# Kernel tuning notes

Hardware: AMD Instinct MI355X
Metric: run time of the kernel (lower is better)

Reference implementation:

```python
import jax, jax.numpy as jnp
import numpy as np

CG_ITER = 10

def _fftc(x):
    # centered orthonormal 2D FFT over last two axes
    ax = (-2, -1)
    return jnp.fft.fftshift(jnp.fft.fft2(jnp.fft.ifftshift(x, axes=ax), axes=ax, norm='ortho'), axes=ax)

def _ifftc(x):
    ax = (-2, -1)
    return jnp.fft.fftshift(jnp.fft.ifft2(jnp.fft.ifftshift(x, axes=ax), axes=ax, norm='ortho'), axes=ax)

def setup_inputs() -> dict:
    key = jax.random.key(0)
    k1, k2, k3, k4, k5 = jax.random.split(key, 5)
    B, C, H, W = 8, 16, 320, 320
    us_image = jax.random.normal(k1, (B, 2, H, W), dtype=jnp.float32)
    reconstruction = jax.random.normal(k2, (B, 2, H, W), dtype=jnp.float32)
    mask = (jax.random.uniform(k3, (B, 1, H, W)) < 0.4).astype(jnp.float32)
    csm_r = jax.random.normal(k4, (B, C, H, W), dtype=jnp.float32)
    csm_i = jax.random.normal(k5, (B, C, H, W), dtype=jnp.float32)
    mu = jnp.full((1,), 0.5, dtype=jnp.float32)
    return {'us_image': us_image, 'reconstruction': reconstruction, 'mask': mask,
            'csm_r': csm_r, 'csm_i': csm_i, 'mu': mu}

def reference(us_image, reconstruction, mask, csm_r, csm_i, mu):
    csm = csm_r + 1j * csm_i                      # [B,C,H,W] complex64
    m = mu[0]
    r = (us_image[:, 0] + 1j * us_image[:, 1]) + m * (reconstruction[:, 0] + 1j * reconstruction[:, 1])  # [B,H,W]
    p = r
    b = jnp.zeros_like(r)
    for _ in range(CG_ITER):
        coil_p = p[:, None, :, :] * csm           # coil projection [B,C,H,W]
        kspace = _fftc(coil_p) * mask             # masked k-space
        q = jnp.sum(_ifftc(kspace) * jnp.conj(csm), axis=1) + m * p  # coil combine + Tikhonov
        rr = jnp.sum(r * jnp.conj(r))
        alpha = rr / jnp.sum(q * jnp.conj(p))
        b = b + alpha * p
        r_new = r - alpha * q
        beta = jnp.sum(r_new * jnp.conj(r_new)) / rr
        p = r_new + beta * p
        r = r_new
    return jnp.stack((b.real, b.imag), axis=1).astype(jnp.float32)  # [B,2,H,W]
```

## Files before the change

### kernel.cpp

```cpp
#include <hip/hip_runtime.h>

#define HW2 320
#define NB 8
#define NC 16
#define NPIX (HW2*HW2)
#define NVEC (NB*NPIX)
#define CGI 10
#define FSCALE (1.0f/102400.0f)

__device__ inline float2 cadd(float2 a, float2 b){return make_float2(a.x+b.x, a.y+b.y);}
__device__ inline float2 csub(float2 a, float2 b){return make_float2(a.x-b.x, a.y-b.y);}
__device__ inline float2 cmul(float2 a, float2 b){return make_float2(a.x*b.x-a.y*b.y, a.x*b.y+a.y*b.x);}
__device__ inline float2 cmulc(float2 a, float2 b){return make_float2(a.x*b.x+a.y*b.y, a.y*b.x-a.x*b.y);}
__device__ inline float2 cscale(float2 a, float s){return make_float2(a.x*s, a.y*s);}
__device__ inline int rev6(int t){ return (int)(__brev((unsigned)t) >> 26); }
__device__ inline float2 shflx2(float2 a, int m){ return make_float2(__shfl_xor(a.x,m,64), __shfl_xor(a.y,m,64)); }
__device__ inline float2 shfl2(float2 a, int l){ return make_float2(__shfl(a.x,l,64), __shfl(a.y,l,64)); }

template<int H>
__device__ inline float2 xsh2t(float2 a) {
  if constexpr (H == 1) {
    return make_float2(
      __int_as_float(__builtin_amdgcn_mov_dpp(__float_as_int(a.x), 0xB1, 0xF, 0xF, true)),
      __int_as_float(__builtin_amdgcn_mov_dpp(__float_as_int(a.y), 0xB1, 0xF, 0xF, true)));
  } else if constexpr (H == 2) {
    return make_float2(
      __int_as_float(__builtin_amdgcn_mov_dpp(__float_as_int(a.x), 0x4E, 0xF, 0xF, true)),
      __int_as_float(__builtin_amdgcn_mov_dpp(__float_as_int(a.y), 0x4E, 0xF, 0xF, true)));
  } else if constexpr (H == 32) {
    return shflx2(a, 32);
  } else {
    constexpr int imm = (H << 10) | 0x1F;
    return make_float2(
      __int_as_float(__builtin_amdgcn_ds_swizzle(__float_as_int(a.x), imm)),
      __int_as_float(__builtin_amdgcn_ds_swizzle(__float_as_int(a.y), imm)));
  }
}

template<int DIR>
__device__ inline void radix5(float2 (&v)[5]) {
  const float c1 = 0.30901699437494745f, s1 = 0.9510565162951535f;
  const float c2 = -0.8090169943749473f, s2 = 0.5877852522924731f;
  float2 t1 = cadd(v[1], v[4]), t2 = csub(v[1], v[4]);
  float2 t3 = cadd(v[2], v[3]), t4 = csub(v[2], v[3]);
  float2 y0 = cadd(v[0], cadd(t1, t3));
  float2 a1 = make_float2(v[0].x + c1*t1.x + c2*t3.x, v[0].y + c1*t1.y + c2*t3.y);
  float2 a2 = make_float2(v[0].x + c2*t1.x + c1*t3.x, v[0].y + c2*t1.y + c1*t3.y);
  float2 b1 = make_float2(s1*t2.x + s2*t4.x, s1*t2.y + s2*t4.y);
  float2 b2 = make_float2(s2*t2.x - s1*t4.x, s2*t2.y - s1*t4.y);
  const float sg = (float)DIR;
  float2 ib1 = make_float2(-sg*b1.y, sg*b1.x);
  float2 ib2 = make_float2(-sg*b2.y, sg*b2.x);
  v[0] = y0;
  v[1] = cadd(a1, ib1); v[4] = csub(a1, ib1);
  v[2] = cadd(a2, ib2); v[3] = csub(a2, ib2);
}

__device__ inline void load_tw(const float2* __restrict__ twg, int t,
                               float2 (&tw5)[4], float2 (&Wf)[6], float (&sg)[6]) {
  #pragma unroll
  for (int q = 1; q < 5; ++q) tw5[q-1] = twg[q*t];
  float2 tw[6];
  tw[0] = twg[5*(t&31)];
  tw[1] = twg[10*(t&15)];
  tw[2] = twg[20*(t&7)];
  tw[3] = twg[40*(t&3)];
  tw[4] = twg[80*(t&1)];
  tw[5] = make_float2(1.f, 0.f);
  #pragma unroll
  for (int s = 0; s < 6; ++s) {
    bool up = (t & (32 >> s)) != 0;
    Wf[s] = up ? tw[s] : make_float2(1.f, 0.f);
    sg[s] = up ? -1.f : 1.f;
  }
}

template<int H, int NCOL>
__device__ inline void bf_fwd(float2 (&v)[NCOL][5], float2 w, float st) {
  #pragma unroll
  for (int q = 0; q < 5; ++q)
    #pragma unroll
    for (int k = 0; k < NCOL; ++k) {
      float2 o = xsh2t<H>(v[k][q]);
      float2 tmp = make_float2(fmaf(st, v[k][q].x, o.x), fmaf(st, v[k][q].y, o.y));
      v[k][q] = cmul(tmp, w);
    }
}
template<int H, int NCOL>
__device__ inline void bf_inv(float2 (&v)[NCOL][5], float2 w, float st) {
  #pragma unroll
  for (int q = 0; q < 5; ++q)
    #pragma unroll
    for (int k = 0; k < NCOL; ++k) {
      float2 mine = cmulc(v[k][q], w);
      float2 o = xsh2t<H>(mine);
      v[k][q] = make_float2(fmaf(st, mine.x, o.x), fmaf(st, mine.y, o.y));
    }
}

template<int NCOL>
__device__ inline void fft320_fwd_r(float2 (&v)[NCOL][5],
                                    const float2 (&tw5)[4], const float2 (&Wf)[6],
                                    const float (&sg)[6]) {
  #pragma unroll
  for (int k = 0; k < NCOL; ++k) radix5<-1>(v[k]);
  #pragma unroll
  for (int q = 1; q < 5; ++q)
    #pragma unroll
    for (int k = 0; k < NCOL; ++k) v[k][q] = cmul(v[k][q], tw5[q-1]);
  bf_fwd<32>(v, Wf[0], sg[0]);
  bf_fwd<16>(v, Wf[1], sg[1]);
  bf_fwd< 8>(v, Wf[2], sg[2]);
  bf_fwd< 4>(v, Wf[3], sg[3]);
  bf_fwd< 2>(v, Wf[4], sg[4]);
  bf_fwd< 1>(v, Wf[5], sg[5]);
}
template<int NCOL>
__device__ inline void fft320_inv_r(float2 (&v)[NCOL][5],
                                    const float2 (&tw5)[4], const float2 (&Wf)[6],
                                    const float (&sg)[6]) {
  bf_inv< 1>(v, Wf[5], sg[5]);
  bf_inv< 2>(v, Wf[4], sg[4]);
  bf_inv< 4>(v, Wf[3], sg[3]);
  bf_inv< 8>(v, Wf[2], sg[2]);
  bf_inv<16>(v, Wf[1], sg[1]);
  bf_inv<32>(v, Wf[0], sg[0]);
  #pragma unroll
  for (int q = 1; q < 5; ++q)
    #pragma unroll
    for (int k = 0; k < NCOL; ++k) v[k][q] = cmulc(v[k][q], tw5[q-1]);
  #pragma unroll
  for (int k = 0; k < NCOL; ++k) radix5<1>(v[k]);
}

__global__ void k_twiddle(float2* tw) {
  int m = blockIdx.x*blockDim.x + threadIdx.x;
  if (m < 320) {
    double a = -2.0 * 3.14159265358979323846 * (double)m / 320.0;
    tw[m] = make_float2((float)cos(a), (float)sin(a));
  }
}

__global__ void k_init(const float* __restrict__ us, const float* __restrict__ rec,
                       const float* __restrict__ mu,
                       float2* r, float2* p, float2* bv) {
  int i = blockIdx.x*blockDim.x + threadIdx.x;
  if (i >= NVEC) return;
  float m = mu[0];
  int b = i / NPIX, hw = i % NPIX;
  float re = us[(size_t)(b*2+0)*NPIX + hw] + m * rec[(size_t)(b*2+0)*NPIX + hw];
  float im = us[(size_t)(b*2+1)*NPIX + hw] + m * rec[(size_t)(b*2+1)*NPIX + hw];
  float2 v = make_float2(re, im);
  r[i] = v; p[i] = v; bv[i] = make_float2(0.f, 0.f);
}

__global__ __launch_bounds__(256) void k_proj_rowfft(
    const float2* __restrict__ pv, const float* __restrict__ csr,
    const float* __restrict__ csi, float2* __restrict__ K,
    const float2* __restrict__ twg, int b0) {
  __shared__ float2 stage[8][320];
  int t = threadIdx.x & 63, w = threadIdx.x >> 6, rt = rev6(t);
  float2 tw5[4], Wf[6]; float sg[6];
  load_tw(twg, t, tw5, Wf, sg);
  int wid = blockIdx.x*4 + w;
  int rp  = wid % (HW2/2);
  int c   = (wid / (HW2/2)) % NC;
  int bl  = wid / ((HW2/2)*NC);
  int b   = b0 + bl;
  int row0 = rp*2;
  const float2* prow = pv + ((size_t)(b*HW2) + row0)*HW2;
  size_t cs = ((size_t)((b*NC + c)*HW2) + row0)*HW2;
  float sgn0 = ((row0 + t) & 1) ? -1.f : 1.f;
  float sgn1 = -sgn0;
  float2 v[2][5];
  #pragma unroll
  for (int j = 0; j < 5; ++j) {
    int n = t + 64*j;
    float2 cv0 = make_float2(csr[cs+n],     csi[cs+n]);
    float2 cv1 = make_float2(csr[cs+HW2+n], csi[cs+HW2+n]);
    v[0][j] = cscale(cmul(prow[n],     cv0), sgn0);
    v[1][j] = cscale(cmul(prow[HW2+n], cv1), sgn1);
  }
  fft320_fwd_r<2>(v, tw5, Wf, sg);
  #pragma unroll
  for (int q = 0; q < 5; ++q) {
    stage[w*2+0][5*rt + q] = v[0][q];
    stage[w*2+1][5*rt + q] = v[1][q];
  }
  float2* Krow = K + ((size_t)((bl*NC + c)*HW2) + row0)*HW2;
  #pragma unroll
  for (int j = 0; j < 5; ++j) {
    Krow[t + 64*j]       = stage[w*2+0][t + 64*j];
    Krow[HW2 + t + 64*j] = stage[w*2+1][t + 64*j];
  }
}

__global__ __launch_bounds__(512, 4) void k_colfft_mask(
    float2* __restrict__ K, const float* __restrict__ mask,
    const float2* __restrict__ twg, int b0) {
  __shared__ float re[320][17];
  __shared__ float im[320][17];
  __shared__ unsigned char mk8[320][20];
  int tile = blockIdx.x % 20;
  int c    = (blockIdx.x/20) % NC;
  int bl   = blockIdx.x/(20*NC);
  int b    = b0 + bl;
  float2* Kimg = K + (size_t)(bl*NC + c)*NPIX;
  const float4* Kimg4 = (const float4*)Kimg;
  const float4* Mimg4 = (const float4*)(mask + (size_t)b*NPIX);
  int t = threadIdx.x & 63, w = threadIdx.x >> 6, rt = rev6(t);
  float2 tw5[4], Wf[6]; float sg[6];
  load_tw(twg, t, tw5, Wf, sg);
  for (int idx = threadIdx.x; idx < 320*8; idx += 512) {
    int rw = idx >> 3, c4 = idx & 7;
    float4 v4 = Kimg4[(size_t)rw*160 + tile*8 + c4];
    re[rw][2*c4+0] = v4.x; im[rw][2*c4+0] = v4.y;
    re[rw][2*c4+1] = v4.z; im[rw][2*c4+1] = v4.w;
  }
  for (int idx = threadIdx.x; idx < 320*4; idx += 512) {
    int rw = idx >> 2, c4 = idx & 3;
    float4 m4 = Mimg4[(size_t)rw*80 + tile*4 + c4];
    mk8[rw][4*c4+0] = (unsigned char)(m4.x != 0.f);
    mk8[rw][4*c4+1] = (unsigned char)(m4.y != 0.f);
    mk8[rw][4*c4+2] = (unsigned char)(m4.z != 0.f);
    mk8[rw][4*c4+3] = (unsigned char)(m4.w != 0.f);
  }
  __syncthreads();
  const int colA = w*2, colB = w*2 + 1;
  float2 v[2][5];
  #pragma unroll
  for (int j = 0; j < 5; ++j) {
    v[0][j] = make_float2(re[t+64*j][colA], im[t+64*j][colA]);
    v[1][j] = make_float2(re[t+64*j][colB], im[t+64*j][colB]);
  }
  fft320_fwd_r<2>(v, tw5, Wf, sg);
  #pragma unroll
  for (int q = 0; q < 5; ++q) {
    int rowk = 5*rt + q;
    float m0 = mk8[rowk][colA] ? FSCALE : 0.f;
    float m1 = mk8[rowk][colB] ? FSCALE : 0.f;
    v[0][q] = cscale(v[0][q], m0);
    v[1][q] = cscale(v[1][q], m1);
  }
  fft320_inv_r<2>(v, tw5, Wf, sg);
  #pragma unroll
  for (int j = 0; j < 5; ++j) {
    re[t+64*j][colA] = v[0][j].x; im[t+64*j][colA] = v[0][j].y;
    re[t+64*j][colB] = v[1][j].x; im[t+64*j][colB] = v[1][j].y;
  }
  __syncthreads();
  float4* Kimg4w = (float4*)Kimg;
  for (int idx = threadIdx.x; idx < 320*8; idx += 512) {
    int rw = idx >> 3, c4 = idx & 7;
    float4 v4;
    v4.x = re[rw][2*c4+0]; v4.y = im[rw][2*c4+0];
    v4.z = re[rw][2*c4+1]; v4.w = im[rw][2*c4+1];
    Kimg4w[(size_t)rw*160 + tile*8 + c4] = v4;
  }
}

__global__ __launch_bounds__(256) void k_irowfft_combine(
    const float2* __restrict__ K, const float* __restrict__ csr,
    const float* __restrict__ csi, const float2* __restrict__ pv,
    float2* __restrict__ qv, const float* __restrict__ mu,
    const float2* __restrict__ twg, int b0) {
  __shared__ float2 rows[4][320];
  int t = threadIdx.x & 63, w = threadIdx.x >> 6, rt = rev6(t);
  float2 tw5[4], Wf[6]; float sg[6];
  load_tw(twg, t, tw5, Wf, sg);
  int row = blockIdx.x % HW2;
  int bl  = blockIdx.x / HW2;
  int b   = b0 + bl;
  float sgn = ((row + t) & 1) ? -1.f : 1.f;
  float2 acc[5];
  #pragma unroll
  for (int j = 0; j < 5; ++j) acc[j] = make_float2(0.f, 0.f);
  #pragma unroll
  for (int half = 0; half < 2; ++half) {
    int c0 = w + 8*half;
    const float2* Kr0 = K + ((size_t)((bl*NC + c0)*HW2) + row)*HW2;
    const float2* Kr1 = Kr0 + (size_t)4*NPIX;
    float2 v[2][5];
    #pragma unroll
    for (int q = 0; q < 5; ++q) { v[0][q] = Kr0[5*t+q]; v[1][q] = Kr1[5*t+q]; }
    #pragma unroll
    for (int q = 0; q < 5; ++q) { v[0][q] = shfl2(v[0][q], rt); v[1][q] = shfl2(v[1][q], rt); }
    fft320_inv_r<2>(v, tw5, Wf, sg);
    size_t cs0 = ((size_t)((b*NC + c0)*HW2) + row)*HW2;
    size_t cs1 = cs0 + (size_t)4*NPIX;
    #pragma unroll
    for (int j = 0; j < 5; ++j) {
      int n = t + 64*j;
      float2 cv0 = make_float2(csr[cs0+n], csi[cs0+n]);
      float2 cv1 = make_float2(csr[cs1+n], csi[cs1+n]);
      acc[j] = cadd(acc[j], cadd(cmulc(v[0][j], cv0), cmulc(v[1][j], cv1)));
    }
  }
  #pragma unroll
  for (int j = 0; j < 5; ++j) rows[w][t+64*j] = cscale(acc[j], sgn);
  __syncthreads();
  float m = mu[0];
  const float* pf = (const float*)(pv + ((size_t)(b*HW2) + row)*HW2);
  float*       qf = (float*)(qv + ((size_t)(b*HW2) + row)*HW2);
  const float* rf = (const float*)rows;
  for (int i = threadIdx.x; i < 640; i += 256) {
    float s = rf[i] + rf[640+i] + rf[1280+i] + rf[1920+i];
    qf[i] = s + m * pf[i];
  }
}

__global__ void k_dot_rr(const float4* __restrict__ r, float2* partials) {
  float s = 0.f;
  for (int i = blockIdx.x*blockDim.x + threadIdx.x; i < NVEC/2; i += gridDim.x*blockDim.x) {
    float4 v = r[i]; s += v.x*v.x + v.y*v.y + v.z*v.z + v.w*v.w;
  }
  __shared__ float buf[4];
  for (int off = 32; off; off >>= 1) s += __shfl_down(s, off, 64);
  int w = threadIdx.x >> 6, t = threadIdx.x & 63;
  if (t == 0) buf[w] = s;
  __syncthreads();
  if (threadIdx.x == 0) partials[blockIdx.x] = make_float2(buf[0]+buf[1]+buf[2]+buf[3], 0.f);
}
__global__ void k_rr_finish(const float2* __restrict__ partials, float2* scal) {
  float s = 0.f;
  for (int i = threadIdx.x; i < 256; i += blockDim.x) s += partials[i].x;
  __shared__ float buf[4];
  for (int off = 32; off; off >>= 1) s += __shfl_down(s, off, 64);
  int w = threadIdx.x >> 6, t = threadIdx.x & 63;
  if (t == 0) buf[w] = s;
  __syncthreads();
  if (threadIdx.x == 0) scal[0] = make_float2(buf[0]+buf[1]+buf[2]+buf[3], 0.f);
}
__global__ void k_dot_pq(const float4* __restrict__ q, const float4* __restrict__ p, float2* partials) {
  float sr = 0.f, si = 0.f;
  for (int i = blockIdx.x*blockDim.x + threadIdx.x; i < NVEC/2; i += gridDim.x*blockDim.x) {
    float4 qq = q[i], pp = p[i];
    sr += qq.x*pp.x + qq.y*pp.y + qq.z*pp.z + qq.w*pp.w;
    si += qq.y*pp.x - qq.x*pp.y + qq.w*pp.z - qq.z*pp.w;
  }
  __shared__ float2 buf[4];
  for (int off = 32; off; off >>= 1) { sr += __shfl_down(sr, off, 64); si += __shfl_down(si, off, 64); }
  int w = threadIdx.x >> 6, t = threadIdx.x & 63;
  if (t == 0) buf[w] = make_float2(sr, si);
  __syncthreads();
  if (threadIdx.x == 0)
    partials[blockIdx.x] = make_float2(buf[0].x+buf[1].x+buf[2].x+buf[3].x,
                                       buf[0].y+buf[1].y+buf[2].y+buf[3].y);
}
__global__ void k_alpha(const float2* __restrict__ partials, float2* scal) {
  float sr = 0.f, si = 0.f;
  for (int i = threadIdx.x; i < 256; i += blockDim.x) { sr += partials[i].x; si += partials[i].y; }
  __shared__ float2 buf[4];
  for (int off = 32; off; off >>= 1) { sr += __shfl_down(sr, off, 64); si += __shfl_down(si, off, 64); }
  int w = threadIdx.x >> 6, t = threadIdx.x & 63;
  if (t == 0) buf[w] = make_float2(sr, si);
  __syncthreads();
  if (threadIdx.x == 0) {
    float pr = buf[0].x+buf[1].x+buf[2].x+buf[3].x;
    float pi = buf[0].y+buf[1].y+buf[2].y+buf[3].y;
    float rr = scal[0].x;
    float d = pr*pr + pi*pi;
    scal[1] = make_float2(rr*pr/d, -rr*pi/d);
  }
}
__global__ void k_update(float4* bv, float4* r, const float4* __restrict__ p,
                         const float4* __restrict__ q, const float2* __restrict__ scal,
                         float2* partials) {
  float2 al = scal[1];
  float s = 0.f;
  for (int i = blockIdx.x*blockDim.x + threadIdx.x; i < NVEC/2; i += gridDim.x*blockDim.x) {
    float4 pp = p[i], qq = q[i], bb = bv[i], rr = r[i];
    bb.x += al.x*pp.x - al.y*pp.y;  bb.y += al.x*pp.y + al.y*pp.x;
    bb.z += al.x*pp.z - al.y*pp.w;  bb.w += al.x*pp.w + al.y*pp.z;
    bv[i] = bb;
    rr.x -= al.x*qq.x - al.y*qq.y;  rr.y -= al.x*qq.y + al.y*qq.x;
    rr.z -= al.x*qq.z - al.y*qq.w;  rr.w -= al.x*qq.w + al.y*qq.z;
    r[i] = rr;
    s += rr.x*rr.x + rr.y*rr.y + rr.z*rr.z + rr.w*rr.w;
  }
  __shared__ float buf[4];
  for (int off = 32; off; off >>= 1) s += __shfl_down(s, off, 64);
  int w = threadIdx.x >> 6, t = threadIdx.x & 63;
  if (t == 0) buf[w] = s;
  __syncthreads();
  if (threadIdx.x == 0) partials[blockIdx.x] = make_float2(buf[0]+buf[1]+buf[2]+buf[3], 0.f);
}
__global__ void k_beta(const float2* __restrict__ partials, float2* scal) {
  float s = 0.f;
  for (int i = threadIdx.x; i < 256; i += blockDim.x) s += partials[i].x;
  __shared__ float buf[4];
  for (int off = 32; off; off >>= 1) s += __shfl_down(s, off, 64);
  int w = threadIdx.x >> 6, t = threadIdx.x & 63;
  if (t == 0) buf[w] = s;
  __syncthreads();
  if (threadIdx.x == 0) {
    float rrnew = buf[0]+buf[1]+buf[2]+buf[3];
    float rrold = scal[0].x;
    scal[2] = make_float2(rrnew/rrold, 0.f);
    scal[0] = make_float2(rrnew, 0.f);
  }
}
__global__ void k_pupdate(float4* p, const float4* __restrict__ r, const float2* __restrict__ scal) {
  float be = scal[2].x;
  for (int i = blockIdx.x*blockDim.x + threadIdx.x; i < NVEC/2; i += gridDim.x*blockDim.x) {
    float4 pp = p[i], rr = r[i];
    pp.x = rr.x + be*pp.x; pp.y = rr.y + be*pp.y;
    pp.z = rr.z + be*pp.z; pp.w = rr.w + be*pp.w;
    p[i] = pp;
  }
}
__global__ void k_output(const float2* __restrict__ bv, float* __restrict__ out) {
  int i = blockIdx.x*blockDim.x + threadIdx.x;
  if (i >= NVEC) return;
  int b = i / NPIX, hw = i % NPIX;
  float2 v = bv[i];
  out[(size_t)(b*2+0)*NPIX + hw] = v.x;
  out[(size_t)(b*2+1)*NPIX + hw] = v.y;
}

extern "C" void kernel_launch(void* const* d_in, const int* in_sizes, int n_in,
                              void* d_out, int out_size, void* d_ws, size_t ws_size,
                              hipStream_t stream) {
  const float* us  = (const float*)d_in[0];
  const float* rec = (const float*)d_in[1];
  const float* msk = (const float*)d_in[2];
  const float* csr = (const float*)d_in[3];
  const float* csi = (const float*)d_in[4];
  const float* mu  = (const float*)d_in[5];
  float* out = (float*)d_out;

  const size_t vecB = (size_t)NVEC * 8;
  int nb = NB;
  while (nb > 1 && ((size_t)nb*NC*NPIX*8 + 4*vecB + 320*8 + 256*8 + 64) > ws_size) nb >>= 1;

  char* w = (char*)d_ws; size_t off = 0;
  float2* K        = (float2*)(w + off); off += (size_t)nb*NC*NPIX*8;
  float2* rv       = (float2*)(w + off); off += vecB;
  float2* pv       = (float2*)(w + off); off += vecB;
  float2* bv       = (float2*)(w + off); off += vecB;
  float2* qv       = (float2*)(w + off); off += vecB;
  float2* twg      = (float2*)(w + off); off += 320*8;
  float2* partials = (float2*)(w + off); off += 256*8;
  float2* scal     = (float2*)(w + off);

  k_twiddle<<<dim3(2), dim3(256), 0, stream>>>(twg);
  k_init<<<dim3(NVEC/256), dim3(256), 0, stream>>>(us, rec, mu, rv, pv, bv);
  k_dot_rr<<<dim3(256), dim3(256), 0, stream>>>((const float4*)rv, partials);
  k_rr_finish<<<dim3(1), dim3(256), 0, stream>>>(partials, scal);

  for (int it = 0; it < CGI; ++it) {
    for (int b0 = 0; b0 < NB; b0 += nb) {
      k_proj_rowfft    <<<dim3(nb*NC*(HW2/2)/4), dim3(256), 0, stream>>>(pv, csr, csi, K, twg, b0);
      k_colfft_mask    <<<dim3(nb*NC*20),        dim3(512), 0, stream>>>(K, msk, twg, b0);
      k_irowfft_combine<<<dim3(nb*HW2),          dim3(256), 0, stream>>>(K, csr, csi, pv, qv, mu, twg, b0);
    }
    k_dot_pq <<<dim3(256), dim3(256), 0, stream>>>((const float4*)qv, (const float4*)pv, partials);
    k_alpha  <<<dim3(1),   dim3(256), 0, stream>>>(partials, scal);
    k_update <<<dim3(256), dim3(256), 0, stream>>>((float4*)bv, (float4*)rv, (const float4*)pv,
                                                   (const float4*)qv, scal, partials);
    k_beta   <<<dim3(1),   dim3(256), 0, stream>>>(partials, scal);
    k_pupdate<<<dim3(256), dim3(256), 0, stream>>>((float4*)pv, (const float4*)rv, scal);
  }
  k_output<<<dim3(NVEC/256), dim3(256), 0, stream>>>(bv, out);
}
```

Before: 1.618 ms.

## Keep k-space rows in digit-reversed order and fold scalar CG reductions into updates

The row FFT now writes its output in the FFT's natural digit-reversed order instead of staging through LDS to unpermute. The inverse row FFT reads that order directly, without shuffles. The mask is pre-permuted once into a byte array so the column pass gets matching column ordering and reads 1-byte values instead of floats. The single-block alpha and beta kernels are removed: each update block redundantly reduces the 256 partials itself, and rr values are stored per iteration in a slot array. This cuts launches and serial tiny kernels per CG iteration, at the cost of a permuted intermediate layout that every stage must agree on.

```diff
diff --git a/kernel.cpp b/kernel.cpp
--- a/kernel.cpp
+++ b/kernel.cpp
@@ -15,7 +15,6 @@
 __device__ inline float2 cscale(float2 a, float s){return make_float2(a.x*s, a.y*s);}
 __device__ inline int rev6(int t){ return (int)(__brev((unsigned)t) >> 26); }
 __device__ inline float2 shflx2(float2 a, int m){ return make_float2(__shfl_xor(a.x,m,64), __shfl_xor(a.y,m,64)); }
-__device__ inline float2 shfl2(float2 a, int l){ return make_float2(__shfl(a.x,l,64), __shfl(a.y,l,64)); }
 
 template<int H>
 __device__ inline float2 xsh2t(float2 a) {
@@ -27,6 +26,10 @@
     return make_float2(
       __int_as_float(__builtin_amdgcn_mov_dpp(__float_as_int(a.x), 0x4E, 0xF, 0xF, true)),
       __int_as_float(__builtin_amdgcn_mov_dpp(__float_as_int(a.y), 0x4E, 0xF, 0xF, true)));
+  } else if constexpr (H == 8) {
+    return make_float2(
+      __int_as_float(__builtin_amdgcn_mov_dpp(__float_as_int(a.x), 0x128, 0xF, 0xF, true)),
+      __int_as_float(__builtin_amdgcn_mov_dpp(__float_as_int(a.y), 0x128, 0xF, 0xF, true)));
   } else if constexpr (H == 32) {
     return shflx2(a, 32);
   } else {
@@ -141,6 +144,15 @@
   }
 }
 
+__global__ void k_maskperm(const float* __restrict__ mask, unsigned char* __restrict__ mp) {
+  int i = blockIdx.x*blockDim.x + threadIdx.x;
+  if (i >= NVEC) return;
+  int p = i % HW2;
+  int rowb = i / HW2;
+  int kw = 5*rev6(p & 63) + (p >> 6);
+  mp[i] = (unsigned char)(mask[(size_t)rowb*HW2 + kw] != 0.f);
+}
+
 __global__ void k_init(const float* __restrict__ us, const float* __restrict__ rec,
                        const float* __restrict__ mu,
                        float2* r, float2* p, float2* bv) {
@@ -158,8 +170,7 @@
     const float2* __restrict__ pv, const float* __restrict__ csr,
     const float* __restrict__ csi, float2* __restrict__ K,
     const float2* __restrict__ twg, int b0) {
-  __shared__ float2 stage[8][320];
-  int t = threadIdx.x & 63, w = threadIdx.x >> 6, rt = rev6(t);
+  int t = threadIdx.x & 63, w = threadIdx.x >> 6;
   float2 tw5[4], Wf[6]; float sg[6];
   load_tw(twg, t, tw5, Wf, sg);
   int wid = blockIdx.x*4 + w;
@@ -182,21 +193,16 @@
     v[1][j] = cscale(cmul(prow[HW2+n], cv1), sgn1);
   }
   fft320_fwd_r<2>(v, tw5, Wf, sg);
+  float2* Krow = K + ((size_t)((bl*NC + c)*HW2) + row0)*HW2;
   #pragma unroll
   for (int q = 0; q < 5; ++q) {
-    stage[w*2+0][5*rt + q] = v[0][q];
-    stage[w*2+1][5*rt + q] = v[1][q];
-  }
-  float2* Krow = K + ((size_t)((bl*NC + c)*HW2) + row0)*HW2;
-  #pragma unroll
-  for (int j = 0; j < 5; ++j) {
-    Krow[t + 64*j]       = stage[w*2+0][t + 64*j];
-    Krow[HW2 + t + 64*j] = stage[w*2+1][t + 64*j];
+    Krow[64*q + t]       = v[0][q];
+    Krow[HW2 + 64*q + t] = v[1][q];
   }
 }
 
 __global__ __launch_bounds__(512, 4) void k_colfft_mask(
-    float2* __restrict__ K, const float* __restrict__ mask,
+    float2* __restrict__ K, const unsigned char* __restrict__ mp,
     const float2* __restrict__ twg, int b0) {
   __shared__ float re[320][17];
   __shared__ float im[320][17];
@@ -207,7 +213,7 @@
   int b    = b0 + bl;
   float2* Kimg = K + (size_t)(bl*NC + c)*NPIX;
   const float4* Kimg4 = (const float4*)Kimg;
-  const float4* Mimg4 = (const float4*)(mask + (size_t)b*NPIX);
+  const uchar4* Mp4   = (const uchar4*)(mp + (size_t)b*NPIX);
   int t = threadIdx.x & 63, w = threadIdx.x >> 6, rt = rev6(t);
   float2 tw5[4], Wf[6]; float sg[6];
   load_tw(twg, t, tw5, Wf, sg);
@@ -219,11 +225,11 @@
   }
   for (int idx = threadIdx.x; idx < 320*4; idx += 512) {
     int rw = idx >> 2, c4 = idx & 3;
-    float4 m4 = Mimg4[(size_t)rw*80 + tile*4 + c4];
-    mk8[rw][4*c4+0] = (unsigned char)(m4.x != 0.f);
-    mk8[rw][4*c4+1] = (unsigned char)(m4.y != 0.f);
-    mk8[rw][4*c4+2] = (unsigned char)(m4.z != 0.f);
-    mk8[rw][4*c4+3] = (unsigned char)(m4.w != 0.f);
+    uchar4 m4 = Mp4[(size_t)rw*80 + tile*4 + c4];
+    mk8[rw][4*c4+0] = m4.x;
+    mk8[rw][4*c4+1] = m4.y;
+    mk8[rw][4*c4+2] = m4.z;
+    mk8[rw][4*c4+3] = m4.w;
   }
   __syncthreads();
   const int colA = w*2, colB = w*2 + 1;
@@ -265,7 +271,7 @@
     float2* __restrict__ qv, const float* __restrict__ mu,
     const float2* __restrict__ twg, int b0) {
   __shared__ float2 rows[4][320];
-  int t = threadIdx.x & 63, w = threadIdx.x >> 6, rt = rev6(t);
+  int t = threadIdx.x & 63, w = threadIdx.x >> 6;
   float2 tw5[4], Wf[6]; float sg[6];
   load_tw(twg, t, tw5, Wf, sg);
   int row = blockIdx.x % HW2;
@@ -282,9 +288,7 @@
     const float2* Kr1 = Kr0 + (size_t)4*NPIX;
     float2 v[2][5];
     #pragma unroll
-    for (int q = 0; q < 5; ++q) { v[0][q] = Kr0[5*t+q]; v[1][q] = Kr1[5*t+q]; }
-    #pragma unroll
-    for (int q = 0; q < 5; ++q) { v[0][q] = shfl2(v[0][q], rt); v[1][q] = shfl2(v[1][q], rt); }
+    for (int q = 0; q < 5; ++q) { v[0][q] = Kr0[64*q + t]; v[1][q] = Kr1[64*q + t]; }
     fft320_inv_r<2>(v, tw5, Wf, sg);
     size_t cs0 = ((size_t)((b*NC + c0)*HW2) + row)*HW2;
     size_t cs1 = cs0 + (size_t)4*NPIX;
@@ -321,7 +325,7 @@
   __syncthreads();
   if (threadIdx.x == 0) partials[blockIdx.x] = make_float2(buf[0]+buf[1]+buf[2]+buf[3], 0.f);
 }
-__global__ void k_rr_finish(const float2* __restrict__ partials, float2* scal) {
+__global__ void k_rr_finish(const float2* __restrict__ partials, float* rrslot) {
   float s = 0.f;
   for (int i = threadIdx.x; i < 256; i += blockDim.x) s += partials[i].x;
   __shared__ float buf[4];
@@ -329,7 +333,7 @@
   int w = threadIdx.x >> 6, t = threadIdx.x & 63;
   if (t == 0) buf[w] = s;
   __syncthreads();
-  if (threadIdx.x == 0) scal[0] = make_float2(buf[0]+buf[1]+buf[2]+buf[3], 0.f);
+  if (threadIdx.x == 0) rrslot[0] = buf[0]+buf[1]+buf[2]+buf[3];
 }
 __global__ void k_dot_pq(const float4* __restrict__ q, const float4* __restrict__ p, float2* partials) {
   float sr = 0.f, si = 0.f;
@@ -347,67 +351,63 @@
     partials[blockIdx.x] = make_float2(buf[0].x+buf[1].x+buf[2].x+buf[3].x,
                                        buf[0].y+buf[1].y+buf[2].y+buf[3].y);
 }
-__global__ void k_alpha(const float2* __restrict__ partials, float2* scal) {
-  float sr = 0.f, si = 0.f;
-  for (int i = threadIdx.x; i < 256; i += blockDim.x) { sr += partials[i].x; si += partials[i].y; }
-  __shared__ float2 buf[4];
-  for (int off = 32; off; off >>= 1) { sr += __shfl_down(sr, off, 64); si += __shfl_down(si, off, 64); }
-  int w = threadIdx.x >> 6, t = threadIdx.x & 63;
-  if (t == 0) buf[w] = make_float2(sr, si);
-  __syncthreads();
-  if (threadIdx.x == 0) {
-    float pr = buf[0].x+buf[1].x+buf[2].x+buf[3].x;
-    float pi = buf[0].y+buf[1].y+buf[2].y+buf[3].y;
-    float rr = scal[0].x;
-    float d = pr*pr + pi*pi;
-    scal[1] = make_float2(rr*pr/d, -rr*pi/d);
-  }
-}
 __global__ void k_update(float4* bv, float4* r, const float4* __restrict__ p,
-                         const float4* __restrict__ q, const float2* __restrict__ scal,
-                         float2* partials) {
-  float2 al = scal[1];
+                         const float4* __restrict__ q,
+                         const float2* __restrict__ partials_pq,
+                         const float* __restrict__ rrslot, int it,
+                         float2* partials_rr) {
+  __shared__ float2 abuf[4];
+  {
+    float2 pq = partials_pq[threadIdx.x];
+    float sr = pq.x, si = pq.y;
+    for (int off = 32; off; off >>= 1) { sr += __shfl_down(sr, off, 64); si += __shfl_down(si, off, 64); }
+    int w0 = threadIdx.x >> 6, t0 = threadIdx.x & 63;
+    if (t0 == 0) abuf[w0] = make_float2(sr, si);
+  }
+  __syncthreads();
+  float pr = abuf[0].x+abuf[1].x+abuf[2].x+abuf[3].x;
+  float pi = abuf[0].y+abuf[1].y+abuf[2].y+abuf[3].y;
+  float rr = rrslot[it];
+  float d = pr*pr + pi*pi;
+  float2 al = make_float2(rr*pr/d, -rr*pi/d);
   float s = 0.f;
   for (int i = blockIdx.x*blockDim.x + threadIdx.x; i < NVEC/2; i += gridDim.x*blockDim.x) {
-    float4 pp = p[i], qq = q[i], bb = bv[i], rr = r[i];
+    float4 pp = p[i], qq = q[i], bb = bv[i], rv = r[i];
     bb.x += al.x*pp.x - al.y*pp.y;  bb.y += al.x*pp.y + al.y*pp.x;
     bb.z += al.x*pp.z - al.y*pp.w;  bb.w += al.x*pp.w + al.y*pp.z;
     bv[i] = bb;
-    rr.x -= al.x*qq.x - al.y*qq.y;  rr.y -= al.x*qq.y + al.y*qq.x;
-    rr.z -= al.x*qq.z - al.y*qq.w;  rr.w -= al.x*qq.w + al.y*qq.z;
-    r[i] = rr;
-    s += rr.x*rr.x + rr.y*rr.y + rr.z*rr.z + rr.w*rr.w;
+    rv.x -= al.x*qq.x - al.y*qq.y;  rv.y -= al.x*qq.y + al.y*qq.x;
+    rv.z -= al.x*qq.z - al.y*qq.w;  rv.w -= al.x*qq.w + al.y*qq.z;
+    r[i] = rv;
+    s += rv.x*rv.x + rv.y*rv.y + rv.z*rv.z + rv.w*rv.w;
   }
   __shared__ float buf[4];
   for (int off = 32; off; off >>= 1) s += __shfl_down(s, off, 64);
   int w = threadIdx.x >> 6, t = threadIdx.x & 63;
   if (t == 0) buf[w] = s;
   __syncthreads();
-  if (threadIdx.x == 0) partials[blockIdx.x] = make_float2(buf[0]+buf[1]+buf[2]+buf[3], 0.f);
-}
-__global__ void k_beta(const float2* __restrict__ partials, float2* scal) {
-  float s = 0.f;
-  for (int i = threadIdx.x; i < 256; i += blockDim.x) s += partials[i].x;
-  __shared__ float buf[4];
-  for (int off = 32; off; off >>= 1) s += __shfl_down(s, off, 64);
-  int w = threadIdx.x >> 6, t = threadIdx.x & 63;
-  if (t == 0) buf[w] = s;
-  __syncthreads();
-  if (threadIdx.x == 0) {
-    float rrnew = buf[0]+buf[1]+buf[2]+buf[3];
-    float rrold = scal[0].x;
-    scal[2] = make_float2(rrnew/rrold, 0.f);
-    scal[0] = make_float2(rrnew, 0.f);
-  }
-}
-__global__ void k_pupdate(float4* p, const float4* __restrict__ r, const float2* __restrict__ scal) {
-  float be = scal[2].x;
+  if (threadIdx.x == 0) partials_rr[blockIdx.x] = make_float2(buf[0]+buf[1]+buf[2]+buf[3], 0.f);
+}
+__global__ void k_pupdate(float4* p, const float4* __restrict__ r,
+                          const float2* __restrict__ partials_rr,
+                          float* rrslot, int it) {
+  __shared__ float bbuf[4];
+  {
+    float s0 = partials_rr[threadIdx.x].x;
+    for (int off = 32; off; off >>= 1) s0 += __shfl_down(s0, off, 64);
+    int w0 = threadIdx.x >> 6, t0 = threadIdx.x & 63;
+    if (t0 == 0) bbuf[w0] = s0;
+  }
+  __syncthreads();
+  float rrnew = bbuf[0]+bbuf[1]+bbuf[2]+bbuf[3];
+  float be = rrnew / rrslot[it];
   for (int i = blockIdx.x*blockDim.x + threadIdx.x; i < NVEC/2; i += gridDim.x*blockDim.x) {
-    float4 pp = p[i], rr = r[i];
-    pp.x = rr.x + be*pp.x; pp.y = rr.y + be*pp.y;
-    pp.z = rr.z + be*pp.z; pp.w = rr.w + be*pp.w;
+    float4 pp = p[i], rv = r[i];
+    pp.x = rv.x + be*pp.x; pp.y = rv.y + be*pp.y;
+    pp.z = rv.z + be*pp.z; pp.w = rv.w + be*pp.w;
     p[i] = pp;
   }
+  if (blockIdx.x == 0 && threadIdx.x == 0) rrslot[it+1] = rrnew;
 }
 __global__ void k_output(const float2* __restrict__ bv, float* __restrict__ out) {
   int i = blockIdx.x*blockDim.x + threadIdx.x;
@@ -431,35 +431,40 @@
 
   const size_t vecB = (size_t)NVEC * 8;
   int nb = NB;
-  while (nb > 1 && ((size_t)nb*NC*NPIX*8 + 4*vecB + 320*8 + 256*8 + 64) > ws_size) nb >>= 1;
+  while (nb > 1 &&
+         ((size_t)nb*NC*NPIX*8 + 4*vecB + 320*8 + 2*256*8 + 64 + NVEC + 64) > ws_size)
+    nb >>= 1;
 
   char* w = (char*)d_ws; size_t off = 0;
-  float2* K        = (float2*)(w + off); off += (size_t)nb*NC*NPIX*8;
-  float2* rv       = (float2*)(w + off); off += vecB;
-  float2* pv       = (float2*)(w + off); off += vecB;
-  float2* bv       = (float2*)(w + off); off += vecB;
-  float2* qv       = (float2*)(w + off); off += vecB;
-  float2* twg      = (float2*)(w + off); off += 320*8;
-  float2* partials = (float2*)(w + off); off += 256*8;
-  float2* scal     = (float2*)(w + off);
-
-  k_twiddle<<<dim3(2), dim3(256), 0, stream>>>(twg);
-  k_init<<<dim3(NVEC/256), dim3(256), 0, stream>>>(us, rec, mu, rv, pv, bv);
-  k_dot_rr<<<dim3(256), dim3(256), 0, stream>>>((const float4*)rv, partials);
-  k_rr_finish<<<dim3(1), dim3(256), 0, stream>>>(partials, scal);
+  float2* K           = (float2*)(w + off); off += (size_t)nb*NC*NPIX*8;
+  float2* rv          = (float2*)(w + off); off += vecB;
+  float2* pv          = (float2*)(w + off); off += vecB;
+  float2* bv          = (float2*)(w + off); off += vecB;
+  float2* qv          = (float2*)(w + off); off += vecB;
+  float2* twg         = (float2*)(w + off); off += 320*8;
+  float2* partials_pq = (float2*)(w + off); off += 256*8;
+  float2* partials_rr = (float2*)(w + off); off += 256*8;
+  float*  rrslot      = (float*)(w + off);  off += 64;
+  unsigned char* mp   = (unsigned char*)(w + off); off += NVEC;
+
+  k_twiddle <<<dim3(2),        dim3(256), 0, stream>>>(twg);
+  k_maskperm<<<dim3(NVEC/256), dim3(256), 0, stream>>>(msk, mp);
+  k_init    <<<dim3(NVEC/256), dim3(256), 0, stream>>>(us, rec, mu, rv, pv, bv);
+  k_dot_rr  <<<dim3(256),      dim3(256), 0, stream>>>((const float4*)rv, partials_rr);
+  k_rr_finish<<<dim3(1),       dim3(256), 0, stream>>>(partials_rr, rrslot);
 
   for (int it = 0; it < CGI; ++it) {
     for (int b0 = 0; b0 < NB; b0 += nb) {
       k_proj_rowfft    <<<dim3(nb*NC*(HW2/2)/4), dim3(256), 0, stream>>>(pv, csr, csi, K, twg, b0);
-      k_colfft_mask    <<<dim3(nb*NC*20),        dim3(512), 0, stream>>>(K, msk, twg, b0);
+      k_colfft_mask    <<<dim3(nb*NC*20),        dim3(512), 0, stream>>>(K, mp, twg, b0);
       k_irowfft_combine<<<dim3(nb*HW2),          dim3(256), 0, stream>>>(K, csr, csi, pv, qv, mu, twg, b0);
     }
-    k_dot_pq <<<dim3(256), dim3(256), 0, stream>>>((const float4*)qv, (const float4*)pv, partials);
-    k_alpha  <<<dim3(1),   dim3(256), 0, stream>>>(partials, scal);
+    k_dot_pq <<<dim3(256), dim3(256), 0, stream>>>((const float4*)qv, (const float4*)pv, partials_pq);
     k_update <<<dim3(256), dim3(256), 0, stream>>>((float4*)bv, (float4*)rv, (const float4*)pv,
-                                                   (const float4*)qv, scal, partials);
-    k_beta   <<<dim3(1),   dim3(256), 0, stream>>>(partials, scal);
-    k_pupdate<<<dim3(256), dim3(256), 0, stream>>>((float4*)pv, (const float4*)rv, scal);
+                                                   (const float4*)qv, partials_pq, rrslot, it,
+                                                   partials_rr);
+    k_pupdate<<<dim3(256), dim3(256), 0, stream>>>((float4*)pv, (const float4*)rv, partials_rr,
+                                                   rrslot, it);
   }
   k_output<<<dim3(NVEC/256), dim3(256), 0, stream>>>(bv, out);
 }
```

New measurement: 1.597 ms. About the same (-1.3%).
